# Optimization experiments

Hardware: AMD Instinct MI355X
Metric: run time of the kernel (lower is better)

Reference implementation:

```python
import jax, jax.numpy as jnp
import numpy as np

N = 50000      # num nodes
E = 800000     # num edges (avg degree 16)
IN = 128       # raw node feature dim
H = 64         # h_dim
L = 2          # num_conv
K = 5          # negative_rate
EPS = 1e-3     # keras BatchNormalization default epsilon


def setup_inputs() -> dict:
    key = jax.random.key(0)
    ks = jax.random.split(key, 12)
    node_feat = jax.random.normal(ks[0], (N, IN), dtype=jnp.float32)
    emb_w = jax.random.normal(ks[1], (IN, H), dtype=jnp.float32) * 0.05
    emb_b = jnp.zeros((H,), dtype=jnp.float32)
    conv_w = jax.random.normal(ks[2], (L, 2 * H, H), dtype=jnp.float32) * 0.05
    conv_b = jnp.zeros((L, H), dtype=jnp.float32)
    bn_gamma = 1.0 + 0.1 * jax.random.normal(ks[3], (L, H), dtype=jnp.float32)
    bn_beta = 0.1 * jax.random.normal(ks[4], (L, H), dtype=jnp.float32)
    bn_mean = 0.1 * jax.random.normal(ks[5], (L, H), dtype=jnp.float32)
    bn_var = jax.random.uniform(ks[6], (L, H), dtype=jnp.float32, minval=0.5, maxval=1.5)
    w_relation = jax.random.normal(ks[7], (1, H), dtype=jnp.float32) * 0.05
    src = jax.random.randint(ks[8], (E,), 0, N, dtype=jnp.int32)
    dst = jax.random.randint(ks[9], (E,), 0, N, dtype=jnp.int32)
    neg_dst = jax.random.randint(ks[10], (E * K,), 0, N, dtype=jnp.int32)
    return dict(node_feat=node_feat, emb_w=emb_w, emb_b=emb_b, conv_w=conv_w,
                conv_b=conv_b, bn_gamma=bn_gamma, bn_beta=bn_beta,
                bn_mean=bn_mean, bn_var=bn_var, w_relation=w_relation,
                src=src, dst=dst, neg_dst=neg_dst)


def reference(node_feat, emb_w, emb_b, conv_w, conv_b, bn_gamma, bn_beta,
              bn_mean, bn_var, w_relation, src, dst, neg_dst):
    # embedding layer (Dense)
    h = node_feat @ emb_w + emb_b  # [N, H]
    for i in range(L):
        # edge message: concat(h[src], h[dst]) @ W + b, split W to avoid [E,2H] buffer
        w_s, w_d = conv_w[i, :H], conv_w[i, H:]
        edge_feat = h[src] @ w_s + h[dst] @ w_d + conv_b[i]  # [E, H]
        # scatter-sum messages to destination nodes (zeros for isolated nodes)
        agg = jax.ops.segment_sum(edge_feat, dst, num_segments=N)  # [N, H]
        # node update: sigmoid(msg) + softplus(h)
        h = jax.nn.sigmoid(agg) + jax.nn.softplus(h)
        # BatchNormalization (inference: moving stats), then relu; dropout inactive
        h = bn_gamma[i] * (h - bn_mean[i]) * jax.lax.rsqrt(bn_var[i] + EPS) + bn_beta[i]
        h = jax.nn.relu(h)
    # link scoring: sum(h_u * h_v * w_relation)
    pos_scores = jnp.sum(h[src] * h[dst] * w_relation, axis=1)  # [E]
    neg_src = jnp.repeat(src, K)  # [E*K]
    # scatter-reorder in original is the identity permutation (pos_e_ids == arange(E))
    neg_scores = jnp.sum(h[neg_src] * h[neg_dst] * w_relation, axis=1)  # [E*K]
    return pos_scores, neg_scores
```

## Files before the change

### kernel.cpp

```cpp
#include <hip/hip_runtime.h>
#include <hip/hip_fp16.h>

#define NV 50000
#define EV 800000
#define INF 128
#define HD 64
#define KNEG 5
#define NB ((NV + 1023) / 1024)

#if defined(__has_builtin)
#if __has_builtin(__builtin_amdgcn_fdot2)
#define HAS_FDOT2 1
#endif
#endif

typedef _Float16 half2r __attribute__((ext_vector_type(2)));

__device__ __forceinline__ float dot2acc(unsigned a, unsigned b, float c) {
#ifdef HAS_FDOT2
  return __builtin_amdgcn_fdot2(__builtin_bit_cast(half2r, a),
                                __builtin_bit_cast(half2r, b), c, false);
#else
  const __half2 ha = *(const __half2*)&a;
  const __half2 hb = *(const __half2*)&b;
  return c + __low2float(ha) * __low2float(hb)
           + __high2float(ha) * __high2float(hb);
#endif
}

__device__ __forceinline__ unsigned packh2(float lo, float hi) {
  return __builtin_bit_cast(unsigned, __floats2half2_rn(lo, hi));
}

__global__ __launch_bounds__(256) void embed_hist_kernel(
    const float* __restrict__ feat, const float* __restrict__ W,
    const float* __restrict__ b, __half* __restrict__ h,
    const int* __restrict__ dst, int* __restrict__ deg,
    unsigned short* __restrict__ rank) {
  __shared__ unsigned sF[4][2][256];
  const int lane = threadIdx.x & 63;
  const int wave = threadIdx.x >> 6;
  unsigned Wh[64];
#pragma unroll
  for (int j = 0; j < 64; j++)
    Wh[j] = packh2(W[(2 * j) * HD + lane], W[(2 * j + 1) * HD + lane]);
  const float bias = b[lane];
  const int nwaves = gridDim.x * 4;
  const int wid = blockIdx.x * 4 + wave;
  const int ngroups = NV / 4;

  int buf = 0;
  int g = wid;
  if (g < ngroups) {
    const float4* gp = (const float4*)(feat + (size_t)g * 512);
    const float4 a0 = gp[lane];
    const float4 a1 = gp[lane + 64];
    uint2 c0, c1;
    c0.x = packh2(a0.x, a0.y); c0.y = packh2(a0.z, a0.w);
    c1.x = packh2(a1.x, a1.y); c1.y = packh2(a1.z, a1.w);
    ((uint2*)sF[wave][0])[lane] = c0;
    ((uint2*)sF[wave][0])[lane + 64] = c1;
  }
  for (; g < ngroups; g += nwaves) {
    const int gn = g + nwaves;
    float4 b0, b1;
    if (gn < ngroups) {
      const float4* gp = (const float4*)(feat + (size_t)gn * 512);
      b0 = gp[lane];
      b1 = gp[lane + 64];
    }
    float acc0 = bias, acc1 = bias, acc2 = bias, acc3 = bias;
    const uint4* F = (const uint4*)sF[wave][buf];
#pragma unroll
    for (int t = 0; t < 16; t++) {
      const uint4 x0 = F[t];
      const uint4 x1 = F[16 + t];
      const uint4 x2 = F[32 + t];
      const uint4 x3 = F[48 + t];
      const unsigned w0 = Wh[4 * t + 0];
      const unsigned w1 = Wh[4 * t + 1];
      const unsigned w2 = Wh[4 * t + 2];
      const unsigned w3 = Wh[4 * t + 3];
      acc0 = dot2acc(x0.x, w0, acc0); acc0 = dot2acc(x0.y, w1, acc0);
      acc0 = dot2acc(x0.z, w2, acc0); acc0 = dot2acc(x0.w, w3, acc0);
      acc1 = dot2acc(x1.x, w0, acc1); acc1 = dot2acc(x1.y, w1, acc1);
      acc1 = dot2acc(x1.z, w2, acc1); acc1 = dot2acc(x1.w, w3, acc1);
      acc2 = dot2acc(x2.x, w0, acc2); acc2 = dot2acc(x2.y, w1, acc2);
      acc2 = dot2acc(x2.z, w2, acc2); acc2 = dot2acc(x2.w, w3, acc2);
      acc3 = dot2acc(x3.x, w0, acc3); acc3 = dot2acc(x3.y, w1, acc3);
      acc3 = dot2acc(x3.z, w2, acc3); acc3 = dot2acc(x3.w, w3, acc3);
    }
    __half* hpo = h + (size_t)g * 256 + lane;
    hpo[0]   = __float2half_rn(acc0);
    hpo[64]  = __float2half_rn(acc1);
    hpo[128] = __float2half_rn(acc2);
    hpo[192] = __float2half_rn(acc3);
    if (gn < ngroups) {
      uint2 c0, c1;
      c0.x = packh2(b0.x, b0.y); c0.y = packh2(b0.z, b0.w);
      c1.x = packh2(b1.x, b1.y); c1.y = packh2(b1.z, b1.w);
      ((uint2*)sF[wave][buf ^ 1])[lane] = c0;
      ((uint2*)sF[wave][buf ^ 1])[lane + 64] = c1;
      buf ^= 1;
    }
  }
  for (int e = blockIdx.x * 256 + threadIdx.x; e < EV; e += gridDim.x * 256) {
    const int r = atomicAdd(&deg[dst[e]], 1);
    rank[e] = (unsigned short)r;
  }
}

__global__ __launch_bounds__(1024) void scan_part_kernel(
    const int* __restrict__ deg, int* __restrict__ off,
    int* __restrict__ bsum) {
  __shared__ int wsum[16];
  const int tid = threadIdx.x;
  const int lane = tid & 63;
  const int w = tid >> 6;
  const int i = blockIdx.x * 1024 + tid;
  const int v = (i < NV) ? deg[i] : 0;
  int s = v;
#pragma unroll
  for (int ofs = 1; ofs < 64; ofs <<= 1) {
    int x = __shfl_up(s, ofs, 64);
    if (lane >= ofs) s += x;
  }
  if (lane == 63) wsum[w] = s;
  __syncthreads();
  if (w == 0) {
    int t2 = (lane < 16) ? wsum[lane] : 0;
#pragma unroll
    for (int ofs = 1; ofs < 16; ofs <<= 1) {
      int x = __shfl_up(t2, ofs, 64);
      if (lane >= ofs) t2 += x;
    }
    if (lane < 16) wsum[lane] = t2;
  }
  __syncthreads();
  const int base = (w > 0) ? wsum[w - 1] : 0;
  if (i < NV) off[i] = base + s - v;
  if (tid == 0) bsum[blockIdx.x] = wsum[15];
}

__global__ __launch_bounds__(1024) void scan_fix_kernel(
    const int* __restrict__ bsum, int* __restrict__ off) {
  __shared__ int sbase, stot;
  const int tid = threadIdx.x;
  const int b = blockIdx.x;
  if (tid == 0) {
    int acc = 0, tot = 0;
    for (int j = 0; j < NB; j++) {
      const int x = bsum[j];
      if (j < b) acc += x;
      tot += x;
    }
    sbase = acc;
    stot = tot;
  }
  __syncthreads();
  const int i = b * 1024 + tid;
  if (i < NV) off[i] += sbase;
  if (b == NB - 1 && tid == 0) off[NV] = stot;
}

__global__ __launch_bounds__(256) void perm_kernel(
    const int* __restrict__ src, const int* __restrict__ dst,
    const unsigned short* __restrict__ rank, const int* __restrict__ off,
    unsigned short* __restrict__ gsrc) {
  const int e = blockIdx.x * 256 + threadIdx.x;
  if (e < EV) {
    const int pos = off[dst[e]] + (int)rank[e];
    gsrc[pos] = (unsigned short)src[e];
  }
}

__global__ __launch_bounds__(256) void aggcomb_kernel(
    const __half* __restrict__ hin, __half* __restrict__ hout,
    const unsigned short* __restrict__ gsrc, const int* __restrict__ off,
    const float* __restrict__ wconv, const float* __restrict__ cb,
    const float* __restrict__ gamma, const float* __restrict__ beta,
    const float* __restrict__ mean, const float* __restrict__ var) {
  __shared__ unsigned sS1[4][4][32];
  __shared__ unsigned sH[4][4][32];
  const int wave = threadIdx.x >> 6;
  const int lane = threadIdx.x & 63;
  const int sub = lane >> 4;
  const int q = lane & 15;
  const int f = lane;
  unsigned Ws2[32], Wd2[32];
#pragma unroll
  for (int j = 0; j < 32; j++) {
    Ws2[j] = packh2(wconv[(2 * j) * HD + f], wconv[(2 * j + 1) * HD + f]);
    Wd2[j] = packh2(wconv[(HD + 2 * j) * HD + f],
                    wconv[(HD + 2 * j + 1) * HD + f]);
  }
  const float cbf = cb[f];
  const float gf = gamma[f];
  const float btf = beta[f];
  const float mf = mean[f];
  const float inv = rsqrtf(var[f] + 1e-3f);
  const uint2* hp = (const uint2*)hin;
  const int wid = blockIdx.x * 4 + wave;
  const int nw = gridDim.x * 4;
  const int ngroups = NV / 4;
  for (int g = wid; g < ngroups; g += nw) {
    const int n0 = g * 4;
    const int n = n0 + sub;
    const int j0 = off[n];
    const int deg = off[n + 1] - j0;
    int dm = deg;
    dm = max(dm, __shfl_xor(dm, 16, 64));
    dm = max(dm, __shfl_xor(dm, 32, 64));
    const uint2 hrv = hp[(size_t)n * 16 + q];
    float4 acc = make_float4(0.f, 0.f, 0.f, 0.f);
    for (int base = 0; base < dm; base += 16) {
      const int e = base + q;
      const int eid = (e < deg) ? (int)gsrc[j0 + e] : NV;
#pragma unroll
      for (int i = 0; i < 16; i++) {
        const int a = __shfl(eid, (sub << 4) | i, 64);
        const uint2 v = hp[(size_t)a * 16 + q];
        const __half2 p0 = *(const __half2*)&v.x;
        const __half2 p1 = *(const __half2*)&v.y;
        acc.x += __low2float(p0);
        acc.y += __high2float(p0);
        acc.z += __low2float(p1);
        acc.w += __high2float(p1);
      }
    }
    {
      uint2 s1p;
      s1p.x = packh2(acc.x, acc.y);
      s1p.y = packh2(acc.z, acc.w);
      ((uint2*)sS1[wave][sub])[q] = s1p;
      ((uint2*)sH[wave][sub])[q] = hrv;
    }
#pragma unroll
    for (int m4 = 0; m4 < 4; m4++) {
      const uint4* s1p = (const uint4*)sS1[wave][m4];
      const uint4* hq = (const uint4*)sH[wave][m4];
      float a1a = 0.f, a1b = 0.f, a2a = 0.f, a2b = 0.f;
#pragma unroll
      for (int t = 0; t < 8; t++) {
        const uint4 xs = s1p[t];
        const uint4 xh = hq[t];
        a1a = dot2acc(xs.x, Ws2[4 * t + 0], a1a);
        a1b = dot2acc(xs.y, Ws2[4 * t + 1], a1b);
        a1a = dot2acc(xs.z, Ws2[4 * t + 2], a1a);
        a1b = dot2acc(xs.w, Ws2[4 * t + 3], a1b);
        a2a = dot2acc(xh.x, Wd2[4 * t + 0], a2a);
        a2b = dot2acc(xh.y, Wd2[4 * t + 1], a2b);
        a2a = dot2acc(xh.z, Wd2[4 * t + 2], a2a);
        a2b = dot2acc(xh.w, Wd2[4 * t + 3], a2b);
      }
      const float a1 = a1a + a1b;
      const float a2 = a2a + a2b;
      const float hvf =
          __half2float(((const __half*)sH[wave][m4])[f]);
      const float d = (float)__shfl(deg, m4 << 4, 64);
      const float agg = a1 + d * a2 + d * cbf;
      const float sig = 1.f / (1.f + __expf(-agg));
      const float sp = fmaxf(hvf, 0.f) + log1pf(__expf(-fabsf(hvf)));
      float x = sig + sp;
      x = gf * (x - mf) * inv + btf;
      hout[(size_t)(n0 + m4) * HD + f] = __float2half_rn(fmaxf(x, 0.f));
    }
  }
}

__global__ __launch_bounds__(256) void score_kernel(
    const __half* __restrict__ hh, const int* __restrict__ src,
    const int* __restrict__ dst, const int* __restrict__ neg_dst,
    const float* __restrict__ wrel, float* __restrict__ out) {
  const int tid = blockIdx.x * 256 + threadIdx.x;
  const int e = tid >> 3;
  const int q = tid & 7;
  if (e >= EV) return;
  const int lane = threadIdx.x & 63;
  const int base8 = lane & 56;
  const float4 w0 = ((const float4*)wrel)[2 * q];
  const float4 w1 = ((const float4*)wrel)[2 * q + 1];
  const __half2 wh0 = __floats2half2_rn(w0.x, w0.y);
  const __half2 wh1 = __floats2half2_rn(w0.z, w0.w);
  const __half2 wh2 = __floats2half2_rn(w1.x, w1.y);
  const __half2 wh3 = __floats2half2_rn(w1.z, w1.w);

  const int* ip = (q == 0) ? (src + e)
                : (q == 1) ? (dst + e)
                           : (neg_dst + (size_t)e * KNEG + min(q - 2, KNEG - 1));
  const int myidx = *ip;
  const int s = __shfl(myidx, base8 + 0, 64);
  const int d = __shfl(myidx, base8 + 1, 64);
  int nd[KNEG];
#pragma unroll
  for (int r = 0; r < KNEG; r++) nd[r] = __shfl(myidx, base8 + 2 + r, 64);

  const uint4* hp = (const uint4*)hh;
  const uint4 sv = hp[(size_t)s * 8 + q];
  const uint4 dv = hp[(size_t)d * 8 + q];
  uint4 nv[KNEG];
#pragma unroll
  for (int r = 0; r < KNEG; r++) nv[r] = hp[(size_t)nd[r] * 8 + q];

  const unsigned au0 = __builtin_bit_cast(unsigned,
      __hmul2(*(const __half2*)&sv.x, wh0));
  const unsigned au1 = __builtin_bit_cast(unsigned,
      __hmul2(*(const __half2*)&sv.y, wh1));
  const unsigned au2 = __builtin_bit_cast(unsigned,
      __hmul2(*(const __half2*)&sv.z, wh2));
  const unsigned au3 = __builtin_bit_cast(unsigned,
      __hmul2(*(const __half2*)&sv.w, wh3));

  float v0 = dot2acc(au3, dv.w,
             dot2acc(au2, dv.z,
             dot2acc(au1, dv.y,
             dot2acc(au0, dv.x, 0.f))));
  float v1, v2, v3, v4, v5;
  {
    float pn[KNEG];
#pragma unroll
    for (int r = 0; r < KNEG; r++) {
      pn[r] = dot2acc(au3, nv[r].w,
              dot2acc(au2, nv[r].z,
              dot2acc(au1, nv[r].y,
              dot2acc(au0, nv[r].x, 0.f))));
    }
    v1 = pn[0]; v2 = pn[1]; v3 = pn[2]; v4 = pn[3]; v5 = pn[4];
  }
  {
    const bool hi = (q & 4) != 0;
    float t0 = hi ? v0 : v4, t1 = hi ? v1 : v5;
    float t2 = hi ? v2 : 0.f, t3 = hi ? v3 : 0.f;
    t0 = __shfl_xor(t0, 4, 64); t1 = __shfl_xor(t1, 4, 64);
    t2 = __shfl_xor(t2, 4, 64); t3 = __shfl_xor(t3, 4, 64);
    v0 = (hi ? v4 : v0) + t0;
    v1 = (hi ? v5 : v1) + t1;
    v2 = (hi ? 0.f : v2) + t2;
    v3 = (hi ? 0.f : v3) + t3;
  }
  {
    const bool hi = (q & 2) != 0;
    float t0 = hi ? v0 : v2, t1 = hi ? v1 : v3;
    t0 = __shfl_xor(t0, 2, 64); t1 = __shfl_xor(t1, 2, 64);
    v0 = (hi ? v2 : v0) + t0;
    v1 = (hi ? v3 : v1) + t1;
  }
  {
    const bool hi = (q & 1) != 0;
    float t0 = hi ? v0 : v1;
    t0 = __shfl_xor(t0, 1, 64);
    v0 = (hi ? v1 : v0) + t0;
  }
  if (q == 0) out[e] = v0;
  else if (q <= KNEG) out[(size_t)EV + (size_t)e * KNEG + (q - 1)] = v0;
}

extern "C" void kernel_launch(void* const* d_in, const int* in_sizes, int n_in,
                              void* d_out, int out_size, void* d_ws, size_t ws_size,
                              hipStream_t stream) {
  const float* node_feat = (const float*)d_in[0];
  const float* emb_w     = (const float*)d_in[1];
  const float* emb_b     = (const float*)d_in[2];
  const float* conv_w    = (const float*)d_in[3];
  const float* conv_b    = (const float*)d_in[4];
  const float* bn_gamma  = (const float*)d_in[5];
  const float* bn_beta   = (const float*)d_in[6];
  const float* bn_mean   = (const float*)d_in[7];
  const float* bn_var    = (const float*)d_in[8];
  const float* w_rel     = (const float*)d_in[9];
  const int*   src       = (const int*)d_in[10];
  const int*   dst       = (const int*)d_in[11];
  const int*   neg_dst   = (const int*)d_in[12];
  float* out = (float*)d_out;

  __half* H0 = (__half*)d_ws;
  __half* H1 = H0 + (size_t)(NV + 1) * HD;
  int*   off  = (int*)(H1 + (size_t)(NV + 1) * HD);
  unsigned short* gsrc = (unsigned short*)(off + (NV + 1));
  int*   bsum = (int*)(gsrc + EV);
  int*   deg  = (int*)H1;
  unsigned short* rank = ((unsigned short*)H1) + 2 * NV;

  hipMemsetAsync(deg, 0, (size_t)NV * sizeof(int), stream);
  hipMemsetAsync(H0 + (size_t)NV * HD, 0, HD * sizeof(__half), stream);
  hipMemsetAsync(H1 + (size_t)NV * HD, 0, HD * sizeof(__half), stream);
  embed_hist_kernel<<<1024, 256, 0, stream>>>(node_feat, emb_w, emb_b, H0,
                                              dst, deg, rank);
  scan_part_kernel<<<NB, 1024, 0, stream>>>(deg, off, bsum);
  scan_fix_kernel<<<NB, 1024, 0, stream>>>(bsum, off);
  perm_kernel<<<(EV + 255) / 256, 256, 0, stream>>>(src, dst, rank, off, gsrc);

  aggcomb_kernel<<<1024, 256, 0, stream>>>(
      H0, H1, gsrc, off, conv_w, conv_b,
      bn_gamma, bn_beta, bn_mean, bn_var);
  aggcomb_kernel<<<1024, 256, 0, stream>>>(
      H1, H0, gsrc, off, conv_w + 2 * HD * HD, conv_b + HD,
      bn_gamma + HD, bn_beta + HD, bn_mean + HD, bn_var + HD);

  score_kernel<<<((size_t)EV * 8 + 255) / 256, 256, 0, stream>>>(
      H0, src, dst, neg_dst, w_rel, out);
}
```

Baseline: 295.3 us.

## Widen gather loads, fold zero-row memsets into kernels, nontemporal score stores

The neighbor-gather loop in the aggregation kernel now loads 16-byte rows per lane, with 8 lanes covering a 64-feature row. Each 16-lane group handles two edges per step, and the two halves are combined with an xor shuffle. This halves the number of gather instructions and shuffles per edge. The two memsets that zero the padding row are removed and the zeroing is done inside the embed and scan_fix kernels, which saves two small launches. Score outputs are written with nontemporal stores. The H1 zero row is written in scan_fix because embed_hist reuses H1 as scratch for deg and rank.

```diff
diff --git a/kernel.cpp b/kernel.cpp
--- a/kernel.cpp
+++ b/kernel.cpp
@@ -40,6 +40,8 @@
   __shared__ unsigned sF[4][2][256];
   const int lane = threadIdx.x & 63;
   const int wave = threadIdx.x >> 6;
+  if (blockIdx.x == 0 && threadIdx.x < 32)
+    ((unsigned*)(h + (size_t)NV * HD))[threadIdx.x] = 0u;
   unsigned Wh[64];
 #pragma unroll
   for (int j = 0; j < 64; j++)
@@ -143,10 +145,12 @@
 }
 
 __global__ __launch_bounds__(1024) void scan_fix_kernel(
-    const int* __restrict__ bsum, int* __restrict__ off) {
+    const int* __restrict__ bsum, int* __restrict__ off,
+    unsigned* __restrict__ h1zrow) {
   __shared__ int sbase, stot;
   const int tid = threadIdx.x;
   const int b = blockIdx.x;
+  if (b == 0 && tid < 32) h1zrow[tid] = 0u;
   if (tid == 0) {
     int acc = 0, tot = 0;
     for (int j = 0; j < NB; j++) {
@@ -186,6 +190,8 @@
   const int lane = threadIdx.x & 63;
   const int sub = lane >> 4;
   const int q = lane & 15;
+  const int r8 = q & 7;
+  const int par = q >> 3;
   const int f = lane;
   unsigned Ws2[32], Wd2[32];
 #pragma unroll
@@ -199,7 +205,7 @@
   const float btf = beta[f];
   const float mf = mean[f];
   const float inv = rsqrtf(var[f] + 1e-3f);
-  const uint2* hp = (const uint2*)hin;
+  const uint4* hp = (const uint4*)hin;
   const int wid = blockIdx.x * 4 + wave;
   const int nw = gridDim.x * 4;
   const int ngroups = NV / 4;
@@ -211,54 +217,61 @@
     int dm = deg;
     dm = max(dm, __shfl_xor(dm, 16, 64));
     dm = max(dm, __shfl_xor(dm, 32, 64));
-    const uint2 hrv = hp[(size_t)n * 16 + q];
-    float4 acc = make_float4(0.f, 0.f, 0.f, 0.f);
+    const uint4 hrv = hp[(size_t)n * 8 + r8];
+    float a0 = 0.f, a1 = 0.f, a2 = 0.f, a3 = 0.f;
+    float a4 = 0.f, a5 = 0.f, a6 = 0.f, a7 = 0.f;
     for (int base = 0; base < dm; base += 16) {
       const int e = base + q;
       const int eid = (e < deg) ? (int)gsrc[j0 + e] : NV;
 #pragma unroll
-      for (int i = 0; i < 16; i++) {
-        const int a = __shfl(eid, (sub << 4) | i, 64);
-        const uint2 v = hp[(size_t)a * 16 + q];
+      for (int i = 0; i < 8; i++) {
+        const int a = __shfl(eid, (sub << 4) | (2 * i + par), 64);
+        const uint4 v = hp[(size_t)a * 8 + r8];
         const __half2 p0 = *(const __half2*)&v.x;
         const __half2 p1 = *(const __half2*)&v.y;
-        acc.x += __low2float(p0);
-        acc.y += __high2float(p0);
-        acc.z += __low2float(p1);
-        acc.w += __high2float(p1);
+        const __half2 p2 = *(const __half2*)&v.z;
+        const __half2 p3 = *(const __half2*)&v.w;
+        a0 += __low2float(p0);  a1 += __high2float(p0);
+        a2 += __low2float(p1);  a3 += __high2float(p1);
+        a4 += __low2float(p2);  a5 += __high2float(p2);
+        a6 += __low2float(p3);  a7 += __high2float(p3);
       }
     }
-    {
-      uint2 s1p;
-      s1p.x = packh2(acc.x, acc.y);
-      s1p.y = packh2(acc.z, acc.w);
-      ((uint2*)sS1[wave][sub])[q] = s1p;
-      ((uint2*)sH[wave][sub])[q] = hrv;
+    a0 += __shfl_xor(a0, 8, 64); a1 += __shfl_xor(a1, 8, 64);
+    a2 += __shfl_xor(a2, 8, 64); a3 += __shfl_xor(a3, 8, 64);
+    a4 += __shfl_xor(a4, 8, 64); a5 += __shfl_xor(a5, 8, 64);
+    a6 += __shfl_xor(a6, 8, 64); a7 += __shfl_xor(a7, 8, 64);
+    if (par == 0) {
+      uint4 s1p;
+      s1p.x = packh2(a0, a1); s1p.y = packh2(a2, a3);
+      s1p.z = packh2(a4, a5); s1p.w = packh2(a6, a7);
+      ((uint4*)sS1[wave][sub])[r8] = s1p;
+      ((uint4*)sH[wave][sub])[r8] = hrv;
     }
 #pragma unroll
     for (int m4 = 0; m4 < 4; m4++) {
       const uint4* s1p = (const uint4*)sS1[wave][m4];
       const uint4* hq = (const uint4*)sH[wave][m4];
-      float a1a = 0.f, a1b = 0.f, a2a = 0.f, a2b = 0.f;
+      float b1a = 0.f, b1b = 0.f, b2a = 0.f, b2b = 0.f;
 #pragma unroll
       for (int t = 0; t < 8; t++) {
         const uint4 xs = s1p[t];
         const uint4 xh = hq[t];
-        a1a = dot2acc(xs.x, Ws2[4 * t + 0], a1a);
-        a1b = dot2acc(xs.y, Ws2[4 * t + 1], a1b);
-        a1a = dot2acc(xs.z, Ws2[4 * t + 2], a1a);
-        a1b = dot2acc(xs.w, Ws2[4 * t + 3], a1b);
-        a2a = dot2acc(xh.x, Wd2[4 * t + 0], a2a);
-        a2b = dot2acc(xh.y, Wd2[4 * t + 1], a2b);
-        a2a = dot2acc(xh.z, Wd2[4 * t + 2], a2a);
-        a2b = dot2acc(xh.w, Wd2[4 * t + 3], a2b);
+        b1a = dot2acc(xs.x, Ws2[4 * t + 0], b1a);
+        b1b = dot2acc(xs.y, Ws2[4 * t + 1], b1b);
+        b1a = dot2acc(xs.z, Ws2[4 * t + 2], b1a);
+        b1b = dot2acc(xs.w, Ws2[4 * t + 3], b1b);
+        b2a = dot2acc(xh.x, Wd2[4 * t + 0], b2a);
+        b2b = dot2acc(xh.y, Wd2[4 * t + 1], b2b);
+        b2a = dot2acc(xh.z, Wd2[4 * t + 2], b2a);
+        b2b = dot2acc(xh.w, Wd2[4 * t + 3], b2b);
       }
-      const float a1 = a1a + a1b;
-      const float a2 = a2a + a2b;
+      const float s1w = b1a + b1b;
+      const float hw = b2a + b2b;
       const float hvf =
           __half2float(((const __half*)sH[wave][m4])[f]);
       const float d = (float)__shfl(deg, m4 << 4, 64);
-      const float agg = a1 + d * a2 + d * cbf;
+      const float agg = s1w + d * hw + d * cbf;
       const float sig = 1.f / (1.f + __expf(-agg));
       const float sp = fmaxf(hvf, 0.f) + log1pf(__expf(-fabsf(hvf)));
       float x = sig + sp;
@@ -351,8 +364,10 @@
     t0 = __shfl_xor(t0, 1, 64);
     v0 = (hi ? v1 : v0) + t0;
   }
-  if (q == 0) out[e] = v0;
-  else if (q <= KNEG) out[(size_t)EV + (size_t)e * KNEG + (q - 1)] = v0;
+  if (q == 0) __builtin_nontemporal_store(v0, &out[e]);
+  else if (q <= KNEG)
+    __builtin_nontemporal_store(
+        v0, &out[(size_t)EV + (size_t)e * KNEG + (q - 1)]);
 }
 
 extern "C" void kernel_launch(void* const* d_in, const int* in_sizes, int n_in,
@@ -382,12 +397,11 @@
   unsigned short* rank = ((unsigned short*)H1) + 2 * NV;
 
   hipMemsetAsync(deg, 0, (size_t)NV * sizeof(int), stream);
-  hipMemsetAsync(H0 + (size_t)NV * HD, 0, HD * sizeof(__half), stream);
-  hipMemsetAsync(H1 + (size_t)NV * HD, 0, HD * sizeof(__half), stream);
   embed_hist_kernel<<<1024, 256, 0, stream>>>(node_feat, emb_w, emb_b, H0,
                                               dst, deg, rank);
   scan_part_kernel<<<NB, 1024, 0, stream>>>(deg, off, bsum);
-  scan_fix_kernel<<<NB, 1024, 0, stream>>>(bsum, off);
+  scan_fix_kernel<<<NB, 1024, 0, stream>>>(bsum, off,
+                                           (unsigned*)(H1 + (size_t)NV * HD));
   perm_kernel<<<(EV + 255) / 256, 256, 0, stream>>>(src, dst, rank, off, gsrc);
 
   aggcomb_kernel<<<1024, 256, 0, stream>>>(
```

Measured after the change: 294.2 us. Within noise of the previous version (-0.4%).
